# Optimization experiments

Measured on AMD Instinct MI355X. Metric: run time of the kernel, lower is better.

The kernel has to match this reference:

```python
import jax, jax.numpy as jnp
import numpy as np

ACTION_DIM = 7
CHUNK_SIZE = 4
INPUT_DIM = ACTION_DIM * CHUNK_SIZE  # 28
HIDDEN = 128
LATENT = 64
NUM_CODES = 512
COMMITMENT_COST = 0.25
BATCH = 262144


def setup_inputs() -> dict:
    key = jax.random.key(0)
    ks = jax.random.split(key, 10)

    def lin_init(k, fan_in, fan_out):
        # torch nn.Linear default: U(-1/sqrt(fan_in), 1/sqrt(fan_in)) for W and b
        bound = 1.0 / np.sqrt(fan_in)
        kw, kb = jax.random.split(k)
        W = jax.random.uniform(kw, (fan_in, fan_out), jnp.float32, -bound, bound)
        b = jax.random.uniform(kb, (fan_out,), jnp.float32, -bound, bound)
        return W, b

    x = jax.random.normal(ks[0], (BATCH, INPUT_DIM), jnp.float32)
    enc_w1, enc_b1 = lin_init(ks[1], INPUT_DIM, HIDDEN)
    enc_w2, enc_b2 = lin_init(ks[2], HIDDEN, LATENT)
    codebook = jax.random.uniform(
        ks[3], (NUM_CODES, LATENT), jnp.float32, -1.0 / NUM_CODES, 1.0 / NUM_CODES
    )
    dec_w1, dec_b1 = lin_init(ks[4], LATENT, HIDDEN)
    dec_w2, dec_b2 = lin_init(ks[5], HIDDEN, INPUT_DIM)
    return {
        "x": x,
        "enc_w1": enc_w1, "enc_b1": enc_b1,
        "enc_w2": enc_w2, "enc_b2": enc_b2,
        "codebook": codebook,
        "dec_w1": dec_w1, "dec_b1": dec_b1,
        "dec_w2": dec_w2, "dec_b2": dec_b2,
    }


def reference(x, enc_w1, enc_b1, enc_w2, enc_b2, codebook,
              dec_w1, dec_b1, dec_w2, dec_b2):
    sg = jax.lax.stop_gradient
    # Encoder: Linear -> ReLU -> Linear
    h = jax.nn.relu(x @ enc_w1 + enc_b1)          # (B, 128)
    z = h @ enc_w2 + enc_b2                       # (B, 64)
    # Nearest-code lookup: ||z||^2 + ||e||^2 - 2 z.e
    z2 = jnp.sum(z * z, axis=1, keepdims=True)    # (B, 1)
    e2 = jnp.sum(codebook * codebook, axis=1)     # (C,)
    ze = z @ codebook.T                           # (B, C) dominant intermediate
    distances = z2 + e2 - 2.0 * ze
    indices = jnp.argmin(distances, axis=1)       # (B,)
    quantized = codebook[indices]                 # (B, 64) gather
    # VQ losses
    codebook_loss = jnp.mean((sg(z) - quantized) ** 2)
    commitment_loss = jnp.mean((z - sg(quantized)) ** 2)
    vq_loss = codebook_loss + COMMITMENT_COST * commitment_loss
    # Straight-through estimator
    z_q = z + sg(quantized - z)
    # Decoder
    hd = jax.nn.relu(z_q @ dec_w1 + dec_b1)       # (B, 128)
    recon = hd @ dec_w2 + dec_b2                  # (B, 28)
    recon_loss = jnp.mean((recon - x) ** 2)
    return recon, recon_loss, vq_loss
```

## Files before the change

kernel.cpp:

```cpp
#include <hip/hip_runtime.h>

#define BATCH   262144
#define IN_DIM  28
#define HID     128
#define LAT     64
#define NCODES  512
#define NBLK    256
#define WVS     16
#define NWAVE   (NBLK * WVS)

#define S1 40
#define S2 136
#define SC 72
#define O_LW1 0
#define O_LW2 5120
#define O_LCB 13824
#define O_LD1 50688
#define O_LD2 59904
#define BLOB_SHORTS 64256
#define BLOB_F32    864
#define BLOB_BYTES  (BLOB_SHORTS * 2 + BLOB_F32 * 4)
#define LDS_BYTES   BLOB_BYTES

typedef short v4s __attribute__((ext_vector_type(4)));
typedef short v8s __attribute__((ext_vector_type(8)));
typedef float v4f __attribute__((ext_vector_type(4)));

union u2v4 { unsigned u[2]; v4s s; };

__device__ __forceinline__ unsigned short f2bf(float f) {
  unsigned u = __float_as_uint(f);
  u += 0x7fffu + ((u >> 16) & 1u);
  return (unsigned short)(u >> 16);
}
__device__ __forceinline__ unsigned pk(float hi, float lo) {
  return __builtin_amdgcn_perm(__float_as_uint(hi), __float_as_uint(lo), 0x07060302u);
}
__device__ __forceinline__ float xf0(unsigned u) { return __uint_as_float(u << 16); }
__device__ __forceinline__ float xf1(unsigned u) { return __uint_as_float(u & 0xFFFF0000u); }

__device__ __forceinline__ v4f mfma16(v4s a, v4s b, v4f c) {
  return __builtin_amdgcn_mfma_f32_16x16x16bf16_1k(a, b, c, 0, 0, 0);
}
__device__ __forceinline__ v4s lo4(v8s v) { return __builtin_shufflevector(v, v, 0, 1, 2, 3); }
__device__ __forceinline__ v4s hi4(v8s v) { return __builtin_shufflevector(v, v, 4, 5, 6, 7); }

__device__ __forceinline__ v4s rlpk(v4f h) {
  u2v4 c;
  c.u[0] = pk(fmaxf(h[1], 0.f), fmaxf(h[0], 0.f));
  c.u[1] = pk(fmaxf(h[3], 0.f), fmaxf(h[2], 0.f));
  return c.s;
}
__device__ __forceinline__ v4s zpk(v4f z) {
  u2v4 c; c.u[0] = pk(z[1], z[0]); c.u[1] = pk(z[3], z[2]); return c.s;
}
__device__ __forceinline__ v4s mkv(unsigned a, unsigned b) {
  u2v4 c; c.u[0] = a; c.u[1] = b; return c.s;
}
__device__ __forceinline__ float kpack(float d, unsigned code) {
  return __uint_as_float((__float_as_uint(d) & 0xFFFFFE00u) | code);
}

__global__ __launch_bounds__(256) void vq_prep(
    const float* __restrict__ ew1, const float* __restrict__ eb1,
    const float* __restrict__ ew2, const float* __restrict__ eb2,
    const float* __restrict__ cb,  const float* __restrict__ dw1,
    const float* __restrict__ db1, const float* __restrict__ dw2,
    const float* __restrict__ db2,
    unsigned short* __restrict__ blob) {
  int i = blockIdx.x * 256 + threadIdx.x;
  float* fb = (float*)(blob + BLOB_SHORTS);
  if (i < O_LW2) {
    int row = i / S1, s = i % S1;
    unsigned short v = 0;
    if (s < 32) {
      int q = s >> 3, r2 = s & 7, j = r2 >> 2, e = r2 & 3;
      int k = j * 16 + q * 4 + e;
      if (k < IN_DIM) v = f2bf(ew1[k * HID + row]);
    }
    blob[i] = v;
  } else if (i < O_LCB) {
    int j2 = i - O_LW2; int row = j2 / S2, s = j2 % S2;
    unsigned short v = 0;
    if (s < 128) {
      int q = s >> 5, r2 = s & 31, j = r2 >> 2, e = r2 & 3;
      int k = j * 16 + q * 4 + e;
      v = f2bf(ew2[k * LAT + row]);
    }
    blob[i] = v;
  } else if (i < O_LD1) {
    int j2 = i - O_LCB; int row = j2 / SC, s = j2 % SC;
    unsigned short v = 0;
    if (s < 64) {
      int q = s >> 4, r2 = s & 15, j = r2 >> 2, e = r2 & 3;
      int k = j * 16 + q * 4 + e;
      v = f2bf(-2.0f * cb[row * LAT + k]);
    }
    blob[i] = v;
  } else if (i < O_LD2) {
    int j2 = i - O_LD1; int row = j2 / SC, s = j2 % SC;
    unsigned short v = 0;
    if (s < 64) {
      int q = s >> 4, r2 = s & 15, j = r2 >> 2, e = r2 & 3;
      int k = j * 16 + q * 4 + e;
      v = f2bf(-0.5f * dw1[k * HID + row]);
    }
    blob[i] = v;
  } else if (i < BLOB_SHORTS) {
    int j2 = i - O_LD2; int row = j2 / S2, s = j2 % S2;
    unsigned short v = 0;
    if (s < 128 && row < IN_DIM) {
      int q = s >> 5, r2 = s & 31, j = r2 >> 2, e = r2 & 3;
      int k = j * 16 + q * 4 + e;
      v = f2bf(dw2[k * IN_DIM + row]);
    }
    blob[i] = v;
  } else if (i < BLOB_SHORTS + 512) {
    int c = i - BLOB_SHORTS;
    float s = 0.f;
    for (int d = 0; d < LAT; ++d) { float v = cb[c * LAT + d]; s += v * v; }
    fb[c] = s;
  } else if (i < BLOB_SHORTS + 640) {
    fb[i - BLOB_SHORTS] = eb1[i - BLOB_SHORTS - 512];
  } else if (i < BLOB_SHORTS + 704) {
    fb[i - BLOB_SHORTS] = eb2[i - BLOB_SHORTS - 640];
  } else if (i < BLOB_SHORTS + 832) {
    fb[i - BLOB_SHORTS] = db1[i - BLOB_SHORTS - 704];
  } else if (i < BLOB_SHORTS + 864) {
    int k = i - BLOB_SHORTS - 832;
    fb[i - BLOB_SHORTS] = (k < IN_DIM) ? db2[k] : 0.f;
  }
}

__device__ __forceinline__ void s12_tile(
    const unsigned short* __restrict__ L, const float* __restrict__ LF,
    int lm, int quad, v4s bxlo, v4s bxhi,
    v4s& zf0, v4s& zf1, v4s& zf2, v4s& zf3, float& z2) {
  const int fw1 = O_LW1 + lm * S1 + quad * 8;
  const int fw2 = O_LW2 + lm * S2 + quad * 32;
  v4f za[4];
#pragma unroll
  for (int nt = 0; nt < 4; ++nt)
    za[nt] = *(const v4f*)&LF[640 + nt * 16 + quad * 4];
#pragma unroll 1
  for (int jp = 0; jp < 4; ++jp) {
    v4s h0, h1;
    {
      v8s w = *(const v8s*)&L[fw1 + (2 * jp) * (16 * S1)];
      v4f sd = *(const v4f*)&LF[512 + (2 * jp) * 16 + quad * 4];
      v4f h = mfma16(lo4(w), bxlo, sd);
      h = mfma16(hi4(w), bxhi, h);
      h0 = rlpk(h);
    }
    {
      v8s w = *(const v8s*)&L[fw1 + (2 * jp + 1) * (16 * S1)];
      v4f sd = *(const v4f*)&LF[512 + (2 * jp + 1) * 16 + quad * 4];
      v4f h = mfma16(lo4(w), bxlo, sd);
      h = mfma16(hi4(w), bxhi, h);
      h1 = rlpk(h);
    }
#pragma unroll
    for (int nt = 0; nt < 4; ++nt) {
      v8s w2 = *(const v8s*)&L[fw2 + nt * (16 * S2) + jp * 8];
      za[nt] = mfma16(lo4(w2), h0, za[nt]);
      za[nt] = mfma16(hi4(w2), h1, za[nt]);
    }
  }
  z2 = za[0][0] * za[0][0] + za[0][1] * za[0][1] + za[0][2] * za[0][2] + za[0][3] * za[0][3]
     + za[1][0] * za[1][0] + za[1][1] * za[1][1] + za[1][2] * za[1][2] + za[1][3] * za[1][3]
     + za[2][0] * za[2][0] + za[2][1] * za[2][1] + za[2][2] * za[2][2] + za[2][3] * za[2][3]
     + za[3][0] * za[3][0] + za[3][1] * za[3][1] + za[3][2] * za[3][2] + za[3][3] * za[3][3];
  zf0 = zpk(za[0]); zf1 = zpk(za[1]); zf2 = zpk(za[2]); zf3 = zpk(za[3]);
}

__device__ __forceinline__ void s56_tile(
    const unsigned short* __restrict__ L, const float* __restrict__ LF,
    int lm, int quad, int code,
    unsigned bxu0, unsigned bxu1, unsigned bxu2, unsigned bxu3,
    float* __restrict__ orow, float& racc) {
  const int fd1 = O_LD1 + lm * SC + quad * 16;
  const int fd2 = O_LD2 + lm * S2 + quad * 32;
  const int g = O_LCB + code * SC + quad * 16;
  v8s q0 = *(const v8s*)&L[g];
  v8s q1 = *(const v8s*)&L[g + 8];
  v4f a6[2];
  a6[0] = *(const v4f*)&LF[832 + quad * 4];
  a6[1] = *(const v4f*)&LF[848 + quad * 4];
#pragma unroll 1
  for (int jp = 0; jp < 4; ++jp) {
    v4s h0, h1;
    {
      int j = 2 * jp;
      v8s d0 = *(const v8s*)&L[fd1 + j * (16 * SC)];
      v8s d1 = *(const v8s*)&L[fd1 + j * (16 * SC) + 8];
      v4f sd = *(const v4f*)&LF[704 + j * 16 + quad * 4];
      v4f h = mfma16(lo4(d0), lo4(q0), sd);
      h = mfma16(hi4(d0), hi4(q0), h);
      h = mfma16(lo4(d1), lo4(q1), h);
      h = mfma16(hi4(d1), hi4(q1), h);
      h0 = rlpk(h);
    }
    {
      int j = 2 * jp + 1;
      v8s d0 = *(const v8s*)&L[fd1 + j * (16 * SC)];
      v8s d1 = *(const v8s*)&L[fd1 + j * (16 * SC) + 8];
      v4f sd = *(const v4f*)&LF[704 + j * 16 + quad * 4];
      v4f h = mfma16(lo4(d0), lo4(q0), sd);
      h = mfma16(hi4(d0), hi4(q0), h);
      h = mfma16(lo4(d1), lo4(q1), h);
      h = mfma16(hi4(d1), hi4(q1), h);
      h1 = rlpk(h);
    }
#pragma unroll
    for (int nt = 0; nt < 2; ++nt) {
      v8s w6 = *(const v8s*)&L[fd2 + nt * (16 * S2) + jp * 8];
      a6[nt] = mfma16(lo4(w6), h0, a6[nt]);
      a6[nt] = mfma16(hi4(w6), h1, a6[nt]);
    }
  }
  *(float4*)(orow + quad * 4) = (float4){a6[0][0], a6[0][1], a6[0][2], a6[0][3]};
  if (quad < 3)
    *(float4*)(orow + 16 + quad * 4) = (float4){a6[1][0], a6[1][1], a6[1][2], a6[1][3]};
  float d;
  d = a6[0][0] - xf0(bxu0); racc += d * d;
  d = a6[0][1] - xf1(bxu0); racc += d * d;
  d = a6[0][2] - xf0(bxu1); racc += d * d;
  d = a6[0][3] - xf1(bxu1); racc += d * d;
  d = a6[1][0] - xf0(bxu2); racc += d * d;
  d = a6[1][1] - xf1(bxu2); racc += d * d;
  d = a6[1][2] - xf0(bxu3); racc += d * d;
  d = a6[1][3] - xf1(bxu3); racc += d * d;
}

__global__ __attribute__((amdgpu_flat_work_group_size(1024, 1024)))
__attribute__((amdgpu_waves_per_eu(4, 4)))
void vq_main(
    const float* __restrict__ x,
    const unsigned short* __restrict__ blob,
    float* __restrict__ out, float* __restrict__ partials) {

  extern __shared__ __align__(16) char smem[];
  const unsigned short* L = (const unsigned short*)smem;
  const float*         LF = (const float*)(smem + BLOB_SHORTS * 2);

  const int tid  = threadIdx.x;
  const int wave = tid >> 6;
  const int lane = tid & 63;
  const int quad = lane >> 4;
  const int lm   = lane & 15;

  {
    const float4* src = (const float4*)blob;
    float4* dst = (float4*)smem;
#pragma unroll
    for (int it = 0; it < 9; ++it) {
      int idx = it * 1024 + tid;
      if (idx < BLOB_BYTES / 16) dst[idx] = src[idx];
    }
  }
  __syncthreads();

  const int rbase = blockIdx.x * 1024 + wave * 64;
  float racc = 0.f, vqacc = 0.f;

#pragma unroll 1
  for (int sw = 0; sw < 2; ++sw) {
    const int r0 = rbase + sw * 32;

    unsigned xa0, xa1, xa2, xa3, xb0, xb1, xb2, xb3;
    {
      const float* xpa = x + (size_t)(r0 + lm) * IN_DIM;
      const float* xpb = x + (size_t)(r0 + 16 + lm) * IN_DIM;
      float4 t = *(const float4*)(xpa + quad * 4);
      xa0 = pk(t.y, t.x); xa1 = pk(t.w, t.z);
      t = (quad < 3) ? *(const float4*)(xpa + 16 + quad * 4) : (float4){0.f, 0.f, 0.f, 0.f};
      xa2 = pk(t.y, t.x); xa3 = pk(t.w, t.z);
      t = *(const float4*)(xpb + quad * 4);
      xb0 = pk(t.y, t.x); xb1 = pk(t.w, t.z);
      t = (quad < 3) ? *(const float4*)(xpb + 16 + quad * 4) : (float4){0.f, 0.f, 0.f, 0.f};
      xb2 = pk(t.y, t.x); xb3 = pk(t.w, t.z);
    }

    v4s zfa0, zfa1, zfa2, zfa3, zfb0, zfb1, zfb2, zfb3;
    float z2a, z2b;
    s12_tile(L, LF, lm, quad, mkv(xa0, xa1), mkv(xa2, xa3), zfa0, zfa1, zfa2, zfa3, z2a);
    __builtin_amdgcn_sched_barrier(0);
    s12_tile(L, LF, lm, quad, mkv(xb0, xb1), mkv(xb2, xb3), zfb0, zfb1, zfb2, zfb3, z2b);
    __builtin_amdgcn_sched_barrier(0);

    const int fcb = O_LCB + lm * SC + quad * 16;
    float bkA = __uint_as_float(0x7f7fffffu);
    float bkB = bkA;
#pragma unroll 2
    for (int ct = 0; ct < 32; ++ct) {
      v8s c0 = *(const v8s*)&L[fcb + ct * (16 * SC)];
      v8s c1 = *(const v8s*)&L[fcb + ct * (16 * SC) + 8];
      v4f sd = *(const v4f*)&LF[ct * 16 + quad * 4];
      v4f dA = mfma16(lo4(c0), zfa0, sd);
      dA = mfma16(hi4(c0), zfa1, dA);
      dA = mfma16(lo4(c1), zfa2, dA);
      dA = mfma16(hi4(c1), zfa3, dA);
      v4f dB = mfma16(lo4(c0), zfb0, sd);
      dB = mfma16(hi4(c0), zfb1, dB);
      dB = mfma16(lo4(c1), zfb2, dB);
      dB = mfma16(hi4(c1), zfb3, dB);
      unsigned cbase = (unsigned)(ct * 16 + quad * 4);
      bkA = fminf(bkA, fminf(fminf(kpack(dA[0], cbase), kpack(dA[1], cbase + 1)),
                             fminf(kpack(dA[2], cbase + 2), kpack(dA[3], cbase + 3))));
      bkB = fminf(bkB, fminf(fminf(kpack(dB[0], cbase), kpack(dB[1], cbase + 1)),
                             fminf(kpack(dB[2], cbase + 2), kpack(dB[3], cbase + 3))));
    }

#pragma unroll
    for (int off = 16; off < 64; off <<= 1) {
      bkA = fminf(bkA, __shfl_xor(bkA, off, 64));
      bkB = fminf(bkB, __shfl_xor(bkB, off, 64));
      z2a += __shfl_xor(z2a, off, 64);
      z2b += __shfl_xor(z2b, off, 64);
    }
    unsigned ka = __float_as_uint(bkA), kb = __float_as_uint(bkB);
    int codeA = (int)(ka & 511u), codeB = (int)(kb & 511u);
    if (quad == 0)
      vqacc += z2a + __uint_as_float(ka & 0xFFFFFE00u)
             + z2b + __uint_as_float(kb & 0xFFFFFE00u);
    __builtin_amdgcn_sched_barrier(0);

    s56_tile(L, LF, lm, quad, codeA, xa0, xa1, xa2, xa3,
             out + (size_t)(r0 + lm) * IN_DIM, racc);
    __builtin_amdgcn_sched_barrier(0);
    s56_tile(L, LF, lm, quad, codeB, xb0, xb1, xb2, xb3,
             out + (size_t)(r0 + 16 + lm) * IN_DIM, racc);
  }

#pragma unroll
  for (int off = 1; off < 64; off <<= 1) {
    racc  += __shfl_xor(racc, off, 64);
    vqacc += __shfl_xor(vqacc, off, 64);
  }
  if (lane == 0) {
    size_t w = (size_t)blockIdx.x * WVS + wave;
    partials[w * 2]     = racc;
    partials[w * 2 + 1] = vqacc;
  }
}

__global__ __launch_bounds__(256) void vq_fin(const float* __restrict__ partials,
                                              float* __restrict__ out) {
  float r = 0.f, v = 0.f;
  for (int i = threadIdx.x; i < NWAVE; i += 256) {
    r += partials[2 * i];
    v += partials[2 * i + 1];
  }
#pragma unroll
  for (int off = 1; off < 64; off <<= 1) {
    r += __shfl_xor(r, off, 64);
    v += __shfl_xor(v, off, 64);
  }
  __shared__ float s[4][2];
  int w = threadIdx.x >> 6;
  if ((threadIdx.x & 63) == 0) { s[w][0] = r; s[w][1] = v; }
  __syncthreads();
  if (threadIdx.x == 0) {
    float R = s[0][0] + s[1][0] + s[2][0] + s[3][0];
    float V = s[0][1] + s[1][1] + s[2][1] + s[3][1];
    out[7340032] = R * (1.0f / 7340032.0f);
    out[7340033] = V * (1.25f / 16777216.0f);
  }
}

extern "C" void kernel_launch(void* const* d_in, const int* in_sizes, int n_in,
                              void* d_out, int out_size, void* d_ws, size_t ws_size,
                              hipStream_t stream) {
  const float* x   = (const float*)d_in[0];
  const float* ew1 = (const float*)d_in[1];
  const float* eb1 = (const float*)d_in[2];
  const float* ew2 = (const float*)d_in[3];
  const float* eb2 = (const float*)d_in[4];
  const float* cb  = (const float*)d_in[5];
  const float* dw1 = (const float*)d_in[6];
  const float* db1 = (const float*)d_in[7];
  const float* dw2 = (const float*)d_in[8];
  const float* db2 = (const float*)d_in[9];

  char* ws = (char*)d_ws;
  unsigned short* blob = (unsigned short*)(ws + 0);
  float* partials = (float*)(ws + 132096);

  float* out = (float*)d_out;

  (void)hipFuncSetAttribute((const void*)vq_main,
                            hipFuncAttributeMaxDynamicSharedMemorySize, LDS_BYTES);

  vq_prep<<<255, 256, 0, stream>>>(ew1, eb1, ew2, eb2, cb, dw1, db1, dw2, db2, blob);
  vq_main<<<NBLK, 1024, LDS_BYTES, stream>>>(x, blob, out, partials);
  vq_fin<<<1, 256, 0, stream>>>(partials, out);
}
```

Measured before the change: 138.2 us.

## Interleave two row-tiles in encoder/decoder MFMA chains and parallelize codebook norms

Fuses the two sequential per-tile encoder and decoder passes into paired functions that process both 16-row tiles together. Each weight fragment loaded from LDS now feeds two independent MFMA chains, which halves the weight LDS reads and gives the scheduler independent work to hide MFMA latency. The prep kernel also computes codebook squared norms with 8 lanes per code and shuffle reduction instead of one thread looping over 64 elements. The cost is higher register pressure under the fixed 4-waves-per-EU limit, which could cause spills.

```diff
diff --git a/kernel.cpp b/kernel.cpp
--- a/kernel.cpp
+++ b/kernel.cpp
@@ -21,6 +21,13 @@
 #define BLOB_F32    864
 #define BLOB_BYTES  (BLOB_SHORTS * 2 + BLOB_F32 * 4)
 #define LDS_BYTES   BLOB_BYTES
+
+#define E2_BASE   BLOB_SHORTS
+#define B1_BASE   (BLOB_SHORTS + 4096)
+#define B2_BASE   (B1_BASE + 128)
+#define DB1_BASE  (B2_BASE + 64)
+#define DB2_BASE  (DB1_BASE + 128)
+#define PREP_END  (DB2_BASE + 32)
 
 typedef short v4s __attribute__((ext_vector_type(4)));
 typedef short v8s __attribute__((ext_vector_type(8)));
@@ -115,121 +122,162 @@
       v = f2bf(dw2[k * IN_DIM + row]);
     }
     blob[i] = v;
-  } else if (i < BLOB_SHORTS + 512) {
-    int c = i - BLOB_SHORTS;
-    float s = 0.f;
-    for (int d = 0; d < LAT; ++d) { float v = cb[c * LAT + d]; s += v * v; }
-    fb[c] = s;
-  } else if (i < BLOB_SHORTS + 640) {
-    fb[i - BLOB_SHORTS] = eb1[i - BLOB_SHORTS - 512];
-  } else if (i < BLOB_SHORTS + 704) {
-    fb[i - BLOB_SHORTS] = eb2[i - BLOB_SHORTS - 640];
-  } else if (i < BLOB_SHORTS + 832) {
-    fb[i - BLOB_SHORTS] = db1[i - BLOB_SHORTS - 704];
-  } else if (i < BLOB_SHORTS + 864) {
-    int k = i - BLOB_SHORTS - 832;
-    fb[i - BLOB_SHORTS] = (k < IN_DIM) ? db2[k] : 0.f;
-  }
-}
-
-__device__ __forceinline__ void s12_tile(
+  } else if (i < B1_BASE) {
+    int j = i - E2_BASE;
+    int c = j >> 3, l = j & 7;
+    const float* p = cb + c * LAT + l * 8;
+    float4 a = *(const float4*)p;
+    float4 b = *(const float4*)(p + 4);
+    float s = a.x * a.x + a.y * a.y + a.z * a.z + a.w * a.w
+            + b.x * b.x + b.y * b.y + b.z * b.z + b.w * b.w;
+    s += __shfl_xor(s, 1, 64);
+    s += __shfl_xor(s, 2, 64);
+    s += __shfl_xor(s, 4, 64);
+    if (l == 0) fb[c] = s;
+  } else if (i < B2_BASE) {
+    fb[512 + (i - B1_BASE)] = eb1[i - B1_BASE];
+  } else if (i < DB1_BASE) {
+    fb[640 + (i - B2_BASE)] = eb2[i - B2_BASE];
+  } else if (i < DB2_BASE) {
+    fb[704 + (i - DB1_BASE)] = db1[i - DB1_BASE];
+  } else if (i < PREP_END) {
+    int k = i - DB2_BASE;
+    fb[832 + k] = (k < IN_DIM) ? db2[k] : 0.f;
+  }
+}
+
+__device__ __forceinline__ void s12_pair(
     const unsigned short* __restrict__ L, const float* __restrict__ LF,
-    int lm, int quad, v4s bxlo, v4s bxhi,
-    v4s& zf0, v4s& zf1, v4s& zf2, v4s& zf3, float& z2) {
+    int lm, int quad,
+    v4s bxa_lo, v4s bxa_hi, v4s bxb_lo, v4s bxb_hi,
+    v4s& zfa0, v4s& zfa1, v4s& zfa2, v4s& zfa3,
+    v4s& zfb0, v4s& zfb1, v4s& zfb2, v4s& zfb3,
+    float& z2a, float& z2b) {
   const int fw1 = O_LW1 + lm * S1 + quad * 8;
   const int fw2 = O_LW2 + lm * S2 + quad * 32;
-  v4f za[4];
-#pragma unroll
-  for (int nt = 0; nt < 4; ++nt)
-    za[nt] = *(const v4f*)&LF[640 + nt * 16 + quad * 4];
+  v4f za[4], zb[4];
+#pragma unroll
+  for (int nt = 0; nt < 4; ++nt) {
+    v4f s = *(const v4f*)&LF[640 + nt * 16 + quad * 4];
+    za[nt] = s; zb[nt] = s;
+  }
 #pragma unroll 1
   for (int jp = 0; jp < 4; ++jp) {
-    v4s h0, h1;
+    v4s hA0, hA1, hB0, hB1;
     {
       v8s w = *(const v8s*)&L[fw1 + (2 * jp) * (16 * S1)];
       v4f sd = *(const v4f*)&LF[512 + (2 * jp) * 16 + quad * 4];
-      v4f h = mfma16(lo4(w), bxlo, sd);
-      h = mfma16(hi4(w), bxhi, h);
-      h0 = rlpk(h);
+      v4f h = mfma16(lo4(w), bxa_lo, sd);
+      h = mfma16(hi4(w), bxa_hi, h);
+      hA0 = rlpk(h);
+      h = mfma16(lo4(w), bxb_lo, sd);
+      h = mfma16(hi4(w), bxb_hi, h);
+      hB0 = rlpk(h);
     }
     {
       v8s w = *(const v8s*)&L[fw1 + (2 * jp + 1) * (16 * S1)];
       v4f sd = *(const v4f*)&LF[512 + (2 * jp + 1) * 16 + quad * 4];
-      v4f h = mfma16(lo4(w), bxlo, sd);
-      h = mfma16(hi4(w), bxhi, h);
-      h1 = rlpk(h);
+      v4f h = mfma16(lo4(w), bxa_lo, sd);
+      h = mfma16(hi4(w), bxa_hi, h);
+      hA1 = rlpk(h);
+      h = mfma16(lo4(w), bxb_lo, sd);
+      h = mfma16(hi4(w), bxb_hi, h);
+      hB1 = rlpk(h);
     }
 #pragma unroll
     for (int nt = 0; nt < 4; ++nt) {
       v8s w2 = *(const v8s*)&L[fw2 + nt * (16 * S2) + jp * 8];
-      za[nt] = mfma16(lo4(w2), h0, za[nt]);
-      za[nt] = mfma16(hi4(w2), h1, za[nt]);
-    }
-  }
-  z2 = za[0][0] * za[0][0] + za[0][1] * za[0][1] + za[0][2] * za[0][2] + za[0][3] * za[0][3]
-     + za[1][0] * za[1][0] + za[1][1] * za[1][1] + za[1][2] * za[1][2] + za[1][3] * za[1][3]
-     + za[2][0] * za[2][0] + za[2][1] * za[2][1] + za[2][2] * za[2][2] + za[2][3] * za[2][3]
-     + za[3][0] * za[3][0] + za[3][1] * za[3][1] + za[3][2] * za[3][2] + za[3][3] * za[3][3];
-  zf0 = zpk(za[0]); zf1 = zpk(za[1]); zf2 = zpk(za[2]); zf3 = zpk(za[3]);
-}
-
-__device__ __forceinline__ void s56_tile(
+      za[nt] = mfma16(lo4(w2), hA0, za[nt]);
+      za[nt] = mfma16(hi4(w2), hA1, za[nt]);
+      zb[nt] = mfma16(lo4(w2), hB0, zb[nt]);
+      zb[nt] = mfma16(hi4(w2), hB1, zb[nt]);
+    }
+  }
+  z2a = za[0][0] * za[0][0] + za[0][1] * za[0][1] + za[0][2] * za[0][2] + za[0][3] * za[0][3]
+      + za[1][0] * za[1][0] + za[1][1] * za[1][1] + za[1][2] * za[1][2] + za[1][3] * za[1][3]
+      + za[2][0] * za[2][0] + za[2][1] * za[2][1] + za[2][2] * za[2][2] + za[2][3] * za[2][3]
+      + za[3][0] * za[3][0] + za[3][1] * za[3][1] + za[3][2] * za[3][2] + za[3][3] * za[3][3];
+  z2b = zb[0][0] * zb[0][0] + zb[0][1] * zb[0][1] + zb[0][2] * zb[0][2] + zb[0][3] * zb[0][3]
+      + zb[1][0] * zb[1][0] + zb[1][1] * zb[1][1] + zb[1][2] * zb[1][2] + zb[1][3] * zb[1][3]
+      + zb[2][0] * zb[2][0] + zb[2][1] * zb[2][1] + zb[2][2] * zb[2][2] + zb[2][3] * zb[2][3]
+      + zb[3][0] * zb[3][0] + zb[3][1] * zb[3][1] + zb[3][2] * zb[3][2] + zb[3][3] * zb[3][3];
+  zfa0 = zpk(za[0]); zfa1 = zpk(za[1]); zfa2 = zpk(za[2]); zfa3 = zpk(za[3]);
+  zfb0 = zpk(zb[0]); zfb1 = zpk(zb[1]); zfb2 = zpk(zb[2]); zfb3 = zpk(zb[3]);
+}
+
+__device__ __forceinline__ void s56_pair(
     const unsigned short* __restrict__ L, const float* __restrict__ LF,
-    int lm, int quad, int code,
-    unsigned bxu0, unsigned bxu1, unsigned bxu2, unsigned bxu3,
-    float* __restrict__ orow, float& racc) {
+    int lm, int quad, int codeA, int codeB,
+    unsigned xa0, unsigned xa1, unsigned xa2, unsigned xa3,
+    unsigned xb0, unsigned xb1, unsigned xb2, unsigned xb3,
+    float* __restrict__ orowA, float* __restrict__ orowB, float& racc) {
   const int fd1 = O_LD1 + lm * SC + quad * 16;
   const int fd2 = O_LD2 + lm * S2 + quad * 32;
-  const int g = O_LCB + code * SC + quad * 16;
-  v8s q0 = *(const v8s*)&L[g];
-  v8s q1 = *(const v8s*)&L[g + 8];
-  v4f a6[2];
-  a6[0] = *(const v4f*)&LF[832 + quad * 4];
-  a6[1] = *(const v4f*)&LF[848 + quad * 4];
+  const int gA = O_LCB + codeA * SC + quad * 16;
+  const int gB = O_LCB + codeB * SC + quad * 16;
+  v8s qa0 = *(const v8s*)&L[gA];
+  v8s qa1 = *(const v8s*)&L[gA + 8];
+  v8s qb0 = *(const v8s*)&L[gB];
+  v8s qb1 = *(const v8s*)&L[gB + 8];
+  v4f a6a[2], a6b[2];
+#pragma unroll
+  for (int nt = 0; nt < 2; ++nt) {
+    v4f s = *(const v4f*)&LF[832 + nt * 16 + quad * 4];
+    a6a[nt] = s; a6b[nt] = s;
+  }
 #pragma unroll 1
   for (int jp = 0; jp < 4; ++jp) {
-    v4s h0, h1;
-    {
-      int j = 2 * jp;
+    v4s hA0, hA1, hB0, hB1;
+#pragma unroll
+    for (int jj = 0; jj < 2; ++jj) {
+      int j = 2 * jp + jj;
       v8s d0 = *(const v8s*)&L[fd1 + j * (16 * SC)];
       v8s d1 = *(const v8s*)&L[fd1 + j * (16 * SC) + 8];
       v4f sd = *(const v4f*)&LF[704 + j * 16 + quad * 4];
-      v4f h = mfma16(lo4(d0), lo4(q0), sd);
-      h = mfma16(hi4(d0), hi4(q0), h);
-      h = mfma16(lo4(d1), lo4(q1), h);
-      h = mfma16(hi4(d1), hi4(q1), h);
-      h0 = rlpk(h);
-    }
-    {
-      int j = 2 * jp + 1;
-      v8s d0 = *(const v8s*)&L[fd1 + j * (16 * SC)];
-      v8s d1 = *(const v8s*)&L[fd1 + j * (16 * SC) + 8];
-      v4f sd = *(const v4f*)&LF[704 + j * 16 + quad * 4];
-      v4f h = mfma16(lo4(d0), lo4(q0), sd);
-      h = mfma16(hi4(d0), hi4(q0), h);
-      h = mfma16(lo4(d1), lo4(q1), h);
-      h = mfma16(hi4(d1), hi4(q1), h);
-      h1 = rlpk(h);
+      v4f h = mfma16(lo4(d0), lo4(qa0), sd);
+      h = mfma16(hi4(d0), hi4(qa0), h);
+      h = mfma16(lo4(d1), lo4(qa1), h);
+      h = mfma16(hi4(d1), hi4(qa1), h);
+      v4s ha = rlpk(h);
+      h = mfma16(lo4(d0), lo4(qb0), sd);
+      h = mfma16(hi4(d0), hi4(qb0), h);
+      h = mfma16(lo4(d1), lo4(qb1), h);
+      h = mfma16(hi4(d1), hi4(qb1), h);
+      v4s hb = rlpk(h);
+      if (jj == 0) { hA0 = ha; hB0 = hb; } else { hA1 = ha; hB1 = hb; }
     }
 #pragma unroll
     for (int nt = 0; nt < 2; ++nt) {
       v8s w6 = *(const v8s*)&L[fd2 + nt * (16 * S2) + jp * 8];
-      a6[nt] = mfma16(lo4(w6), h0, a6[nt]);
-      a6[nt] = mfma16(hi4(w6), h1, a6[nt]);
-    }
-  }
-  *(float4*)(orow + quad * 4) = (float4){a6[0][0], a6[0][1], a6[0][2], a6[0][3]};
-  if (quad < 3)
-    *(float4*)(orow + 16 + quad * 4) = (float4){a6[1][0], a6[1][1], a6[1][2], a6[1][3]};
+      a6a[nt] = mfma16(lo4(w6), hA0, a6a[nt]);
+      a6a[nt] = mfma16(hi4(w6), hA1, a6a[nt]);
+      a6b[nt] = mfma16(lo4(w6), hB0, a6b[nt]);
+      a6b[nt] = mfma16(hi4(w6), hB1, a6b[nt]);
+    }
+  }
+  *(float4*)(orowA + quad * 4) = (float4){a6a[0][0], a6a[0][1], a6a[0][2], a6a[0][3]};
+  *(float4*)(orowB + quad * 4) = (float4){a6b[0][0], a6b[0][1], a6b[0][2], a6b[0][3]};
+  if (quad < 3) {
+    *(float4*)(orowA + 16 + quad * 4) = (float4){a6a[1][0], a6a[1][1], a6a[1][2], a6a[1][3]};
+    *(float4*)(orowB + 16 + quad * 4) = (float4){a6b[1][0], a6b[1][1], a6b[1][2], a6b[1][3]};
+  }
   float d;
-  d = a6[0][0] - xf0(bxu0); racc += d * d;
-  d = a6[0][1] - xf1(bxu0); racc += d * d;
-  d = a6[0][2] - xf0(bxu1); racc += d * d;
-  d = a6[0][3] - xf1(bxu1); racc += d * d;
-  d = a6[1][0] - xf0(bxu2); racc += d * d;
-  d = a6[1][1] - xf1(bxu2); racc += d * d;
-  d = a6[1][2] - xf0(bxu3); racc += d * d;
-  d = a6[1][3] - xf1(bxu3); racc += d * d;
+  d = a6a[0][0] - xf0(xa0); racc += d * d;
+  d = a6a[0][1] - xf1(xa0); racc += d * d;
+  d = a6a[0][2] - xf0(xa1); racc += d * d;
+  d = a6a[0][3] - xf1(xa1); racc += d * d;
+  d = a6a[1][0] - xf0(xa2); racc += d * d;
+  d = a6a[1][1] - xf1(xa2); racc += d * d;
+  d = a6a[1][2] - xf0(xa3); racc += d * d;
+  d = a6a[1][3] - xf1(xa3); racc += d * d;
+  d = a6b[0][0] - xf0(xb0); racc += d * d;
+  d = a6b[0][1] - xf1(xb0); racc += d * d;
+  d = a6b[0][2] - xf0(xb1); racc += d * d;
+  d = a6b[0][3] - xf1(xb1); racc += d * d;
+  d = a6b[1][0] - xf0(xb2); racc += d * d;
+  d = a6b[1][1] - xf1(xb2); racc += d * d;
+  d = a6b[1][2] - xf0(xb3); racc += d * d;
+  d = a6b[1][3] - xf1(xb3); racc += d * d;
 }
 
 __global__ __attribute__((amdgpu_flat_work_group_size(1024, 1024)))
@@ -283,9 +331,9 @@
 
     v4s zfa0, zfa1, zfa2, zfa3, zfb0, zfb1, zfb2, zfb3;
     float z2a, z2b;
-    s12_tile(L, LF, lm, quad, mkv(xa0, xa1), mkv(xa2, xa3), zfa0, zfa1, zfa2, zfa3, z2a);
-    __builtin_amdgcn_sched_barrier(0);
-    s12_tile(L, LF, lm, quad, mkv(xb0, xb1), mkv(xb2, xb3), zfb0, zfb1, zfb2, zfb3, z2b);
+    s12_pair(L, LF, lm, quad,
+             mkv(xa0, xa1), mkv(xa2, xa3), mkv(xb0, xb1), mkv(xb2, xb3),
+             zfa0, zfa1, zfa2, zfa3, zfb0, zfb1, zfb2, zfb3, z2a, z2b);
     __builtin_amdgcn_sched_barrier(0);
 
     const int fcb = O_LCB + lm * SC + quad * 16;
@@ -325,11 +373,11 @@
              + z2b + __uint_as_float(kb & 0xFFFFFE00u);
     __builtin_amdgcn_sched_barrier(0);
 
-    s56_tile(L, LF, lm, quad, codeA, xa0, xa1, xa2, xa3,
-             out + (size_t)(r0 + lm) * IN_DIM, racc);
+    s56_pair(L, LF, lm, quad, codeA, codeB,
+             xa0, xa1, xa2, xa3, xb0, xb1, xb2, xb3,
+             out + (size_t)(r0 + lm) * IN_DIM,
+             out + (size_t)(r0 + 16 + lm) * IN_DIM, racc);
     __builtin_amdgcn_sched_barrier(0);
-    s56_tile(L, LF, lm, quad, codeB, xb0, xb1, xb2, xb3,
-             out + (size_t)(r0 + 16 + lm) * IN_DIM, racc);
   }
 
 #pragma unroll
@@ -391,7 +439,8 @@
   (void)hipFuncSetAttribute((const void*)vq_main,
                             hipFuncAttributeMaxDynamicSharedMemorySize, LDS_BYTES);
 
-  vq_prep<<<255, 256, 0, stream>>>(ew1, eb1, ew2, eb2, cb, dw1, db1, dw2, db2, blob);
+  vq_prep<<<(PREP_END + 255) / 256, 256, 0, stream>>>(
+      ew1, eb1, ew2, eb2, cb, dw1, db1, dw2, db2, blob);
   vq_main<<<NBLK, 1024, LDS_BYTES, stream>>>(x, blob, out, partials);
   vq_fin<<<1, 256, 0, stream>>>(partials, out);
 }
```

New measurement: 134.5 us. 1.03x faster.
